# Performance work log

Hardware: AMD Instinct MI355X
Metric: run time of the kernel (lower is better)

The kernel has to match this reference:

```python
import jax, jax.numpy as jnp
import numpy as np

N_NODES = 8192


def _gcn_norm(edge_index, num_nodes):
    # PyG GCNConv default: add self-loops, symmetric normalization.
    src, dst = edge_index[0], edge_index[1]
    loop = jnp.arange(num_nodes, dtype=src.dtype)
    src = jnp.concatenate([src, loop])
    dst = jnp.concatenate([dst, loop])
    deg = jax.ops.segment_sum(jnp.ones_like(dst, dtype=jnp.float32), dst,
                              num_segments=num_nodes)
    dis = jnp.where(deg > 0, jax.lax.rsqrt(jnp.maximum(deg, 1.0)), 0.0)
    norm = dis[src] * dis[dst]  # [E + N]
    return src, dst, norm


def _gcn_conv(x, W, b, src, dst, norm, num_nodes):
    h = x @ W                           # [N, F_out] dense GEMM
    msg = h[src] * norm[:, None]        # gather + scale, [E+N, F_out]
    out = jax.ops.segment_sum(msg, dst, num_segments=num_nodes)  # scatter-add
    return out + b


def setup_inputs() -> dict:
    key = jax.random.key(0)
    ks = jax.random.split(key, 8)
    N, E, F_in, H1, H2, F_out = N_NODES, 65536, 512, 4096, 1024, 10
    x = jax.random.normal(ks[0], (N, F_in), dtype=jnp.float32)
    edge_index = jax.random.randint(ks[1], (2, E), 0, N, dtype=jnp.int64)
    # Glorot-ish scaled weights
    W1 = jax.random.normal(ks[2], (F_in, H1), dtype=jnp.float32) * (1.0 / np.sqrt(F_in))
    b1 = jnp.zeros((H1,), dtype=jnp.float32)
    W2 = jax.random.normal(ks[3], (H1, H2), dtype=jnp.float32) * (1.0 / np.sqrt(H1))
    b2 = jnp.zeros((H2,), dtype=jnp.float32)
    W3 = jax.random.normal(ks[4], (H2, F_out), dtype=jnp.float32) * (1.0 / np.sqrt(H2))
    b3 = jnp.zeros((F_out,), dtype=jnp.float32)
    return {"x": x, "W1": W1, "b1": b1, "W2": W2, "b2": b2,
            "W3": W3, "b3": b3, "edge_index": edge_index}


def reference(x, W1, b1, W2, b2, W3, b3, edge_index):
    N = N_NODES
    src, dst, norm = _gcn_norm(edge_index, N)
    h = _gcn_conv(x.astype(jnp.float32), W1, b1, src, dst, norm, N)
    h = jax.nn.relu(h)  # dropout is identity in eval mode
    h = _gcn_conv(h, W2, b2, src, dst, norm, N)
    h = jax.nn.relu(h)
    h = _gcn_conv(h, W3, b3, src, dst, norm, N)
    return jax.nn.log_softmax(h, axis=1)
```

## Files before the change

kernel.cpp:

```cpp
#include <hip/hip_runtime.h>
#include <math.h>

#define N_NODES 8192
#define N_EDGES 65536
#define F_IN    512
#define HID1    4096
#define HID2    1024
#define F_OUT   10
#define H3_STRIDE 16
#define W3B_STRIDE 1032

typedef __bf16 bf16x8 __attribute__((ext_vector_type(8)));
typedef float floatx4 __attribute__((ext_vector_type(4)));
typedef float floatx16 __attribute__((ext_vector_type(16)));

static __device__ __forceinline__ unsigned short f2bf(float f) {
    union { float f; unsigned u; } v; v.f = f;
    unsigned r = v.u + 0x7fffu + ((v.u >> 16) & 1u);
    return (unsigned short)(r >> 16);
}
static __device__ __forceinline__ float bf2f(unsigned short u) {
    union { unsigned u; float f; } v; v.u = ((unsigned)u) << 16;
    return v.f;
}
static __device__ __forceinline__ void unpack8(uint4 r, float* f) {
    union { unsigned u; float v; } c;
    c.u = r.x << 16;          f[0] = c.v;
    c.u = r.x & 0xffff0000u;  f[1] = c.v;
    c.u = r.y << 16;          f[2] = c.v;
    c.u = r.y & 0xffff0000u;  f[3] = c.v;
    c.u = r.z << 16;          f[4] = c.v;
    c.u = r.z & 0xffff0000u;  f[5] = c.v;
    c.u = r.w << 16;          f[6] = c.v;
    c.u = r.w & 0xffff0000u;  f[7] = c.v;
}
static __device__ __forceinline__ uint4 pack8(const float* f) {
    uint4 o;
    o.x = (unsigned)f2bf(f[0]) | ((unsigned)f2bf(f[1]) << 16);
    o.y = (unsigned)f2bf(f[2]) | ((unsigned)f2bf(f[3]) << 16);
    o.z = (unsigned)f2bf(f[4]) | ((unsigned)f2bf(f[5]) << 16);
    o.w = (unsigned)f2bf(f[6]) | ((unsigned)f2bf(f[7]) << 16);
    return o;
}

__global__ __launch_bounds__(1024) void hist_scan_kernel(
        const int* __restrict__ ei, int* __restrict__ deg,
        int* __restrict__ row_ptr, int* __restrict__ cnt) {
    __shared__ int hist[N_NODES];
    __shared__ int sums[1024];
    int t = threadIdx.x;
#pragma unroll
    for (int i = 0; i < 8; i++) hist[t + i * 1024] = 0;
    __syncthreads();
    const int4* ei4 = (const int4*)(ei + N_EDGES);
#pragma unroll
    for (int i = 0; i < 16; i++) {
        int4 d4 = ei4[i * 1024 + t];
        atomicAdd(&hist[d4.x], 1);
        atomicAdd(&hist[d4.y], 1);
        atomicAdd(&hist[d4.z], 1);
        atomicAdd(&hist[d4.w], 1);
    }
    __syncthreads();
    int base = t * 8;
    int local[8], run = 0;
#pragma unroll
    for (int i = 0; i < 8; i++) {
        int dv = hist[base + i];
        deg[base + i] = dv;
        cnt[base + i] = 0;
        local[i] = run; run += dv;
    }
    sums[t] = run;
    __syncthreads();
    for (int off = 1; off < 1024; off <<= 1) {
        int val = (t >= off) ? sums[t - off] : 0;
        __syncthreads();
        sums[t] += val;
        __syncthreads();
    }
    int offset = (t == 0) ? 0 : sums[t - 1];
#pragma unroll
    for (int i = 0; i < 8; i++) row_ptr[base + i] = offset + local[i];
    if (t == 1023) row_ptr[N_NODES] = sums[1023];
}

static __device__ __forceinline__ void transpose_body(
        const float* __restrict__ W, unsigned short* __restrict__ Wt,
        int K, int N, int k0, int n0, int tid, float (*t)[33]) {
    int c = tid & 31, r8 = tid >> 5;
#pragma unroll
    for (int i = 0; i < 4; i++) {
        int r = r8 + i * 8;
        t[r][c] = W[(size_t)(k0 + r) * N + n0 + c];
    }
    __syncthreads();
#pragma unroll
    for (int i = 0; i < 4; i++) {
        int r = r8 + i * 8;
        Wt[(size_t)(n0 + r) * K + k0 + c] = f2bf(t[c][r]);
    }
}

__global__ __launch_bounds__(256) void megaprep_kernel(
        const int* __restrict__ ei, const int* __restrict__ deg,
        const int* __restrict__ row_ptr, int* __restrict__ cnt,
        int* __restrict__ csr_src, float* __restrict__ csr_w,
        const float* __restrict__ x, unsigned short* __restrict__ xb,
        const float* __restrict__ W1, unsigned short* __restrict__ W1t,
        const float* __restrict__ W2, unsigned short* __restrict__ W2t,
        const float* __restrict__ W3, unsigned short* __restrict__ w3b) {
    __shared__ float t[32][33];
    int b = blockIdx.x, tid = threadIdx.x;
    if (b < 256) {
        int e = b * 256 + tid;
        int s = ei[e];
        int d = ei[N_EDGES + e];
        int slot = row_ptr[d] + atomicAdd(&cnt[d], 1);
        csr_src[slot] = s;
        csr_w[slot] = rsqrtf((float)((deg[s] + 1) * (deg[d] + 1)));
    } else if (b < 4352) {
        int i = (b - 256) * 256 + tid;
        float4 a = ((const float4*)x)[i];
        ushort4 o;
        o.x = f2bf(a.x); o.y = f2bf(a.y); o.z = f2bf(a.z); o.w = f2bf(a.w);
        ((ushort4*)xb)[i] = o;
    } else if (b < 6400) {
        int bb = b - 4352;
        transpose_body(W1, W1t, F_IN, HID1, (bb >> 7) * 32, (bb & 127) * 32, tid, t);
    } else if (b < 10496) {
        int bb = b - 6400;
        transpose_body(W2, W2t, HID1, HID2, (bb >> 5) * 32, (bb & 31) * 32, tid, t);
    } else {
        for (int i = tid; i < HID2 * F_OUT; i += 256) {
            int k = i / F_OUT, c = i % F_OUT;
            w3b[c * W3B_STRIDE + k] = f2bf(W3[i]);
        }
    }
}

__global__ __launch_bounds__(256) void agg1_kernel(
        const unsigned short* __restrict__ xb, const int* __restrict__ row_ptr,
        const int* __restrict__ csr_src, const float* __restrict__ csr_w,
        const int* __restrict__ deg, unsigned short* __restrict__ out) {
    int v = blockIdx.x * 4 + (threadIdx.x >> 6);
    int t = threadIdx.x & 63;
    const uint4* xp = (const uint4*)xb;
    float sw = 1.0f / (float)(deg[v] + 1);
    float acc[8], tmp[8];
    unpack8(xp[(size_t)v * 64 + t], tmp);
#pragma unroll
    for (int j = 0; j < 8; j++) acc[j] = sw * tmp[j];
    int e = row_ptr[v], end = row_ptr[v + 1];
    for (; e + 4 <= end; e += 4) {
        int s0 = csr_src[e], s1 = csr_src[e + 1];
        int s2 = csr_src[e + 2], s3 = csr_src[e + 3];
        float w0 = csr_w[e], w1 = csr_w[e + 1];
        float w2 = csr_w[e + 2], w3 = csr_w[e + 3];
        float f0[8], f1[8], f2[8], f3[8];
        unpack8(xp[(size_t)s0 * 64 + t], f0);
        unpack8(xp[(size_t)s1 * 64 + t], f1);
        unpack8(xp[(size_t)s2 * 64 + t], f2);
        unpack8(xp[(size_t)s3 * 64 + t], f3);
#pragma unroll
        for (int j = 0; j < 8; j++)
            acc[j] += w0 * f0[j] + w1 * f1[j] + w2 * f2[j] + w3 * f3[j];
    }
    for (; e < end; e++) {
        int s = csr_src[e];
        float w = csr_w[e];
        float f0[8];
        unpack8(xp[(size_t)s * 64 + t], f0);
#pragma unroll
        for (int j = 0; j < 8; j++) acc[j] += w * f0[j];
    }
    ((uint4*)out)[(size_t)v * 64 + t] = pack8(acc);
}

__global__ __launch_bounds__(256) void agg2_gemm3_kernel(
        const unsigned short* __restrict__ h, const int* __restrict__ row_ptr,
        const int* __restrict__ csr_src, const float* __restrict__ csr_w,
        const int* __restrict__ deg, const float* __restrict__ b2,
        const unsigned short* __restrict__ w3b, float* __restrict__ H3) {
    __shared__ unsigned short w3s[F_OUT * W3B_STRIDE];
    __shared__ float red[4][F_OUT];
    int tid = threadIdx.x;
    for (int i = tid; i < F_OUT * W3B_STRIDE; i += 256) w3s[i] = w3b[i];
    __syncthreads();
    int half = tid >> 7;
    int t = tid & 127;
    int v = blockIdx.x * 2 + half;
    const uint4* hp = (const uint4*)h;
    float sw = 1.0f / (float)(deg[v] + 1);
    float acc[8], tmp[8];
    unpack8(hp[(size_t)v * 128 + t], tmp);
#pragma unroll
    for (int j = 0; j < 8; j++) acc[j] = sw * tmp[j];
    int e = row_ptr[v], end = row_ptr[v + 1];
    for (; e + 4 <= end; e += 4) {
        int s0 = csr_src[e], s1 = csr_src[e + 1];
        int s2 = csr_src[e + 2], s3 = csr_src[e + 3];
        float w0 = csr_w[e], w1 = csr_w[e + 1];
        float w2 = csr_w[e + 2], w3 = csr_w[e + 3];
        float f0[8], f1[8], f2[8], f3[8];
        unpack8(hp[(size_t)s0 * 128 + t], f0);
        unpack8(hp[(size_t)s1 * 128 + t], f1);
        unpack8(hp[(size_t)s2 * 128 + t], f2);
        unpack8(hp[(size_t)s3 * 128 + t], f3);
#pragma unroll
        for (int j = 0; j < 8; j++)
            acc[j] += w0 * f0[j] + w1 * f1[j] + w2 * f2[j] + w3 * f3[j];
    }
    for (; e < end; e++) {
        int s = csr_src[e];
        float w = csr_w[e];
        float f0[8];
        unpack8(hp[(size_t)s * 128 + t], f0);
#pragma unroll
        for (int j = 0; j < 8; j++) acc[j] += w * f0[j];
    }
    float4 b4a = ((const float4*)b2)[t * 2];
    float4 b4b = ((const float4*)b2)[t * 2 + 1];
    acc[0] = fmaxf(acc[0] + b4a.x, 0.0f); acc[1] = fmaxf(acc[1] + b4a.y, 0.0f);
    acc[2] = fmaxf(acc[2] + b4a.z, 0.0f); acc[3] = fmaxf(acc[3] + b4a.w, 0.0f);
    acc[4] = fmaxf(acc[4] + b4b.x, 0.0f); acc[5] = fmaxf(acc[5] + b4b.y, 0.0f);
    acc[6] = fmaxf(acc[6] + b4b.z, 0.0f); acc[7] = fmaxf(acc[7] + b4b.w, 0.0f);

    float partial[F_OUT];
#pragma unroll
    for (int c = 0; c < F_OUT; c++) {
        float wf[8];
        unpack8(*(const uint4*)&w3s[c * W3B_STRIDE + t * 8], wf);
        partial[c] = acc[0] * wf[0] + acc[1] * wf[1] + acc[2] * wf[2] + acc[3] * wf[3]
                   + acc[4] * wf[4] + acc[5] * wf[5] + acc[6] * wf[6] + acc[7] * wf[7];
    }
#pragma unroll
    for (int c = 0; c < F_OUT; c++) {
#pragma unroll
        for (int off = 32; off > 0; off >>= 1)
            partial[c] += __shfl_xor(partial[c], off, 64);
    }
    int wave = tid >> 6, lane = tid & 63;
    if (lane == 0) {
#pragma unroll
        for (int c = 0; c < F_OUT; c++) red[wave][c] = partial[c];
    }
    __syncthreads();
    if (tid < 2 * F_OUT) {
        int hh = tid / F_OUT, c = tid % F_OUT;
        H3[(size_t)(blockIdx.x * 2 + hh) * H3_STRIDE + c] =
            red[hh * 2][c] + red[hh * 2 + 1][c];
    }
}

#define P8_OFF(R_, lc_) ((((R_) >> 2) * 128) + (((((R_) & 3) << 2) | (lc_)) ^ (((R_) >> 2) & 3)) * 8)

#define Q4_STAGE(Lbuf_, base_, k0_) do {                                       \
    unsigned short* L_ = (Lbuf_);                                              \
    _Pragma("unroll")                                                          \
    for (int j = 0; j < 2; j++) {                                              \
        int sl = j * 512 + tid;                                                \
        int s4 = sl >> 4, cs = sl & 15;                                        \
        int csp = cs ^ (s4 & 3);                                               \
        int grow = s4 * 4 + (csp >> 2);                                        \
        int gcol = (csp & 3) * 8;                                              \
        __builtin_amdgcn_global_load_lds(                                      \
            (const __attribute__((address_space(1))) void*)((base_) + (size_t)grow * K + (k0_) + gcol), \
            (__attribute__((address_space(3))) void*)(&L_[sl * 8]), 16, 0, 0); \
    }                                                                          \
} while (0)

#define P8_STAGE(mat_, kh_, dd_, base_, k0_) \
    Q4_STAGE(lds + ((dd_) * 4 + (mat_) * 2 + (kh_)) * 8192, base_, (k0_) + (kh_) * 32)

#define P8_MAIN_LOOP(NT_)                                                      \
    P8_STAGE(0, 0, 0, Abase, 0);                                               \
    P8_STAGE(1, 0, 0, Bbase, 0);                                               \
    P8_STAGE(0, 1, 0, Abase, 0);                                               \
    P8_STAGE(1, 1, 0, Bbase, 0);                                               \
    asm volatile("s_waitcnt vmcnt(4)" ::: "memory");                           \
    __builtin_amdgcn_s_barrier();                                              \
    for (int t = 0; t < (NT_); t++) {                                          \
        int d = t & 1, dn = d ^ 1;                                             \
        int k1 = (t + 1) * 64;                                                 \
        _Pragma("unroll")                                                      \
        for (int kk = 0; kk < 4; kk++) {                                       \
            if (kk == 2) {                                                     \
                if (t + 1 < (NT_))                                             \
                    asm volatile("s_waitcnt vmcnt(4)" ::: "memory");           \
                else                                                           \
                    asm volatile("s_waitcnt vmcnt(0)" ::: "memory");           \
                __builtin_amdgcn_s_barrier();                                  \
            }                                                                  \
            int kh = kk >> 1;                                                  \
            int lc0 = (kk & 1) * 2 + lhalf;                                    \
            const unsigned short* Ak = lds + (d * 4 + kh) * 8192;              \
            const unsigned short* Bk = lds + (d * 4 + 2 + kh) * 8192;          \
            bf16x8 af[4], bfr[2];                                              \
            _Pragma("unroll")                                                  \
            for (int mt = 0; mt < 4; mt++) {                                   \
                int R = wm * 128 + mt * 32 + lrow;                             \
                af[mt] = *(const bf16x8*)&Ak[P8_OFF(R, lc0)];                  \
            }                                                                  \
            _Pragma("unroll")                                                  \
            for (int nt = 0; nt < 2; nt++) {                                   \
                int R = wn * 64 + nt * 32 + lrow;                              \
                bfr[nt] = *(const bf16x8*)&Bk[P8_OFF(R, lc0)];                 \
            }                                                                  \
            if (t + 1 < (NT_)) {                                               \
                if (kk == 0)      P8_STAGE(0, 0, dn, Abase, k1);               \
                else if (kk == 1) P8_STAGE(1, 0, dn, Bbase, k1);               \
                else if (kk == 2) P8_STAGE(0, 1, dn, Abase, k1);               \
                else              P8_STAGE(1, 1, dn, Bbase, k1);               \
            }                                                                  \
            __builtin_amdgcn_s_barrier();                                      \
            __builtin_amdgcn_s_setprio(1);                                     \
            _Pragma("unroll")                                                  \
            for (int mt = 0; mt < 4; mt++)                                     \
                _Pragma("unroll")                                              \
                for (int nt = 0; nt < 2; nt++)                                 \
                    acc[mt][nt] = __builtin_amdgcn_mfma_f32_32x32x16_bf16(     \
                        af[mt], bfr[nt], acc[mt][nt], 0, 0, 0);                \
            __builtin_amdgcn_s_setprio(0);                                     \
            if (kk == 0 || kk == 2) __builtin_amdgcn_s_barrier();              \
        }                                                                      \
        asm volatile("s_waitcnt vmcnt(4)" ::: "memory");                       \
        __builtin_amdgcn_s_barrier();                                          \
    }

__global__ __launch_bounds__(512, 2) void gemm1_pipe8_kernel(
        const unsigned short* __restrict__ A,
        const unsigned short* __restrict__ Bt,
        const float* __restrict__ bias,
        unsigned short* __restrict__ C) {
    __shared__ unsigned short lds[65536];
    const int K = F_IN, N = HID1;
    int tid = threadIdx.x;
    int wave = tid >> 6, lane = tid & 63;
    int wm = wave >> 2, wn = wave & 3;
    int lrow = lane & 31, lhalf = lane >> 5;

    int b = blockIdx.x;
    int GN = HID1 >> 8;
    int ntile = (b >> 3) % GN;
    int mtile = ((b >> 3) / GN) * 8 + (b & 7);
    int m0 = mtile * 256, n0 = ntile * 256;

    const unsigned short* Abase = A + (size_t)m0 * K;
    const unsigned short* Bbase = Bt + (size_t)n0 * K;

    floatx16 acc[4][2] = {};
    P8_MAIN_LOOP(8)

#pragma unroll
    for (int mt = 0; mt < 4; mt++) {
#pragma unroll
        for (int nt = 0; nt < 2; nt++) {
            int col = n0 + wn * 64 + nt * 32 + lrow;
            float bv = bias[col];
#pragma unroll
            for (int reg = 0; reg < 16; reg++) {
                int row = m0 + wm * 128 + mt * 32 + (reg & 3) + 8 * (reg >> 2) + 4 * lhalf;
                float v = fmaxf(acc[mt][nt][reg] + bv, 0.0f);
                C[(size_t)row * N + col] = f2bf(v);
            }
        }
    }
}

__global__ __launch_bounds__(512, 2) void gemm2_q4v2_split_kernel(
        const unsigned short* __restrict__ A,
        const unsigned short* __restrict__ Bt,
        unsigned short* __restrict__ Ca,
        unsigned short* __restrict__ Cb) {
    __shared__ unsigned short lds[65536];
    const int K = HID1;
    const int N = HID2;
    int tid = threadIdx.x;
    int wave = tid >> 6, lane = tid & 63;
    int wm = wave >> 2, wn = wave & 3;
    int lrow = lane & 31, lhalf = lane >> 5;

    int b = blockIdx.x;
    int u = b >> 3;
    int col = u & 7;
    int mtile = (u >> 3) * 8 + (b & 7);
    int ntile = col >> 1;
    int ksp = col & 1;
    int m0 = mtile * 256, n0 = ntile * 256;
    int koff = ksp * (HID1 / 2);

    const unsigned short* Abase = A + (size_t)m0 * K + koff;
    const unsigned short* Bbase = Bt + (size_t)n0 * K + koff;
    unsigned short* Cout = ksp ? Cb : Ca;

    floatx16 acc[4][2] = {};
    const int NT = (HID1 / 2) >> 5;

    Q4_STAGE(lds + 0 * 16384, Abase, 0);  Q4_STAGE(lds + 0 * 16384 + 8192, Bbase, 0);
    Q4_STAGE(lds + 1 * 16384, Abase, 32); Q4_STAGE(lds + 1 * 16384 + 8192, Bbase, 32);
    Q4_STAGE(lds + 2 * 16384, Abase, 64); Q4_STAGE(lds + 2 * 16384 + 8192, Bbase, 64);
    asm volatile("s_waitcnt vmcnt(8)" ::: "memory");
    __builtin_amdgcn_s_barrier();

    for (int t = 0; t < NT; t++) {
        const unsigned short* Ak = lds + (size_t)(t & 3) * 16384;
        const unsigned short* Bk = Ak + 8192;
        unsigned short* Lnext = lds + (size_t)((t + 3) & 3) * 16384;
        int k3 = (t + 3) * 32;
        if (t + 3 < NT) {
            Q4_STAGE(Lnext, Abase, k3);
            Q4_STAGE(Lnext + 8192, Bbase, k3);
        }
        bf16x8 af[2][4], bfr[2][2];
#pragma unroll
        for (int kk = 0; kk < 2; kk++) {
            int lc0 = kk * 2 + lhalf;
#pragma unroll
            for (int mt = 0; mt < 4; mt++) {
                int R = wm * 128 + mt * 32 + lrow;
                af[kk][mt] = *(const bf16x8*)&Ak[P8_OFF(R, lc0)];
            }
#pragma unroll
            for (int nt = 0; nt < 2; nt++) {
                int R = wn * 64 + nt * 32 + lrow;
                bfr[kk][nt] = *(const bf16x8*)&Bk[P8_OFF(R, lc0)];
            }
        }
        __builtin_amdgcn_s_setprio(1);
#pragma unroll
        for (int kk = 0; kk < 2; kk++)
#pragma unroll
            for (int mt = 0; mt < 4; mt++)
#pragma unroll
                for (int nt = 0; nt < 2; nt++)
                    acc[mt][nt] = __builtin_amdgcn_mfma_f32_32x32x16_bf16(
                        af[kk][mt], bfr[kk][nt], acc[mt][nt], 0, 0, 0);
        __builtin_amdgcn_s_setprio(0);
        if (t + 3 < NT)
            asm volatile("s_waitcnt vmcnt(8)" ::: "memory");
        else if (t + 2 < NT)
            asm volatile("s_waitcnt vmcnt(4)" ::: "memory");
        else if (t + 1 < NT)
            asm volatile("s_waitcnt vmcnt(0)" ::: "memory");
        __builtin_amdgcn_s_barrier();
    }

#pragma unroll
    for (int mt = 0; mt < 4; mt++) {
#pragma unroll
        for (int nt = 0; nt < 2; nt++) {
            int colc = n0 + wn * 64 + nt * 32 + lrow;
#pragma unroll
            for (int reg = 0; reg < 16; reg++) {
                int row = m0 + wm * 128 + mt * 32 + (reg & 3) + 8 * (reg >> 2) + 4 * lhalf;
                Cout[(size_t)row * N + colc] = f2bf(acc[mt][nt][reg]);
            }
        }
    }
}

__global__ __launch_bounds__(256) void merge_kernel(
        const unsigned short* __restrict__ Ca, unsigned short* __restrict__ Cb) {
    const uint4* a4 = (const uint4*)Ca;
    uint4* b4 = (uint4*)Cb;
    int base = blockIdx.x * 1024 + threadIdx.x;
#pragma unroll
    for (int j = 0; j < 4; j++) {
        int i = base + j * 256;
        float fa[8], fb[8];
        unpack8(a4[i], fa);
        unpack8(b4[i], fb);
#pragma unroll
        for (int k = 0; k < 8; k++) fa[k] += fb[k];
        b4[i] = pack8(fa);
    }
}

__global__ void final_kernel(const float* __restrict__ h3, const int* __restrict__ row_ptr,
                             const int* __restrict__ csr_src, const float* __restrict__ csr_w,
                             const int* __restrict__ deg, const float* __restrict__ b3,
                             float* __restrict__ out) {
    int v = blockIdx.x * blockDim.x + threadIdx.x;
    if (v >= N_NODES) return;
    const float4* h4 = (const float4*)h3;
    float sw = 1.0f / (float)(deg[v] + 1);
    float a[12];
    *(float4*)&a[0] = h4[v * 4];
    *(float4*)&a[4] = h4[v * 4 + 1];
    *(float4*)&a[8] = h4[v * 4 + 2];
    float acc[F_OUT];
#pragma unroll
    for (int c = 0; c < F_OUT; c++) acc[c] = b3[c] + sw * a[c];
    int end = row_ptr[v + 1];
    for (int e = row_ptr[v]; e < end; e++) {
        int s = csr_src[e];
        float w = csr_w[e];
        float bsrc[12];
        *(float4*)&bsrc[0] = h4[s * 4];
        *(float4*)&bsrc[4] = h4[s * 4 + 1];
        *(float4*)&bsrc[8] = h4[s * 4 + 2];
#pragma unroll
        for (int c = 0; c < F_OUT; c++) acc[c] += w * bsrc[c];
    }
    float m = acc[0];
#pragma unroll
    for (int c = 1; c < F_OUT; c++) m = fmaxf(m, acc[c]);
    float ssum = 0.0f;
#pragma unroll
    for (int c = 0; c < F_OUT; c++) ssum += expf(acc[c] - m);
    float l = logf(ssum);
#pragma unroll
    for (int c = 0; c < F_OUT; c++) out[v * F_OUT + c] = acc[c] - m - l;
}

extern "C" void kernel_launch(void* const* d_in, const int* in_sizes, int n_in,
                              void* d_out, int out_size, void* d_ws, size_t ws_size,
                              hipStream_t stream) {
    const float* x  = (const float*)d_in[0];
    const float* W1 = (const float*)d_in[1];
    const float* b1 = (const float*)d_in[2];
    const float* W2 = (const float*)d_in[3];
    const float* b2 = (const float*)d_in[4];
    const float* W3 = (const float*)d_in[5];
    const float* b3 = (const float*)d_in[6];
    const int*   ei = (const int*)d_in[7];
    float* out = (float*)d_out;

    char* p = (char*)d_ws;
    int*   deg     = (int*)p;    p += N_NODES * 4;
    int*   cnt     = (int*)p;    p += N_NODES * 4;
    int*   row_ptr = (int*)p;    p += 33024;
    int*   csr_src = (int*)p;    p += N_EDGES * 4;
    float* csr_w   = (float*)p;  p += N_EDGES * 4;
    float* h3      = (float*)p;  p += N_NODES * H3_STRIDE * 4;
    unsigned short* w3b = (unsigned short*)p; p += (F_OUT * W3B_STRIDE * 2 + 255) / 256 * 256;
    unsigned short* xb    = (unsigned short*)p; p += (size_t)N_NODES * F_IN * 2;
    unsigned short* agg_x = (unsigned short*)p; p += (size_t)N_NODES * F_IN * 2;
    unsigned short* W1t   = (unsigned short*)p; p += (size_t)HID1 * F_IN * 2;
    unsigned short* W2t   = (unsigned short*)p; p += (size_t)HID2 * HID1 * 2;
    unsigned short* h1    = (unsigned short*)p; p += (size_t)N_NODES * HID1 * 2;
    unsigned short* h2pre = (unsigned short*)p; p += (size_t)N_NODES * HID2 * 2;
    unsigned short* h2a = xb;

    hist_scan_kernel<<<1, 1024, 0, stream>>>(ei, deg, row_ptr, cnt);
    megaprep_kernel<<<10497, 256, 0, stream>>>(ei, deg, row_ptr, cnt, csr_src, csr_w,
                                               x, xb, W1, W1t, W2, W2t, W3, w3b);

    agg1_kernel<<<N_NODES / 4, 256, 0, stream>>>(xb, row_ptr, csr_src, csr_w, deg, agg_x);
    gemm1_pipe8_kernel<<<(N_NODES / 256) * (HID1 / 256), 512, 0, stream>>>(
        agg_x, W1t, b1, h1);

    gemm2_q4v2_split_kernel<<<256, 512, 0, stream>>>(h1, W2t, h2a, h2pre);
    merge_kernel<<<1024, 256, 0, stream>>>(h2a, h2pre);

    agg2_gemm3_kernel<<<N_NODES / 2, 256, 0, stream>>>(h2pre, row_ptr, csr_src, csr_w,
                                                       deg, b2, w3b, h3);

    final_kernel<<<N_NODES / 256, 256, 0, stream>>>(h3, row_ptr, csr_src, csr_w, deg, b3, out);
}
```

Before: 287.2 us.

## Slice feature dimension in aggregation kernels and interleave GEMM2 prefetch with MFMA

The two gather-aggregation kernels now split each node's feature row into column slices handled by separate blocks. Each lane loads one 32-bit pair instead of a 16-byte vector, which multiplies the number of blocks and the memory-level parallelism for the irregular gathers. The fused layer-3 projection now reads W3 directly into registers, writes per-slice partial sums, and adds a small reduce kernel; this removes the W3 prep and the LDS staging. The GEMM2 loop also issues its next-stage global prefetch inside the kk loop between the fragment loads and the MFMAs to overlap better, at the cost of narrower loads and an extra launch plus partial-sum traffic.

```diff
diff --git a/kernel.cpp b/kernel.cpp
--- a/kernel.cpp
+++ b/kernel.cpp
@@ -8,20 +8,14 @@
 #define HID2    1024
 #define F_OUT   10
 #define H3_STRIDE 16
-#define W3B_STRIDE 1032
 
 typedef __bf16 bf16x8 __attribute__((ext_vector_type(8)));
-typedef float floatx4 __attribute__((ext_vector_type(4)));
 typedef float floatx16 __attribute__((ext_vector_type(16)));
 
 static __device__ __forceinline__ unsigned short f2bf(float f) {
     union { float f; unsigned u; } v; v.f = f;
     unsigned r = v.u + 0x7fffu + ((v.u >> 16) & 1u);
     return (unsigned short)(r >> 16);
-}
-static __device__ __forceinline__ float bf2f(unsigned short u) {
-    union { unsigned u; float f; } v; v.u = ((unsigned)u) << 16;
-    return v.f;
 }
 static __device__ __forceinline__ void unpack8(uint4 r, float* f) {
     union { unsigned u; float v; } c;
@@ -108,8 +102,7 @@
         int* __restrict__ csr_src, float* __restrict__ csr_w,
         const float* __restrict__ x, unsigned short* __restrict__ xb,
         const float* __restrict__ W1, unsigned short* __restrict__ W1t,
-        const float* __restrict__ W2, unsigned short* __restrict__ W2t,
-        const float* __restrict__ W3, unsigned short* __restrict__ w3b) {
+        const float* __restrict__ W2, unsigned short* __restrict__ W2t) {
     __shared__ float t[32][33];
     int b = blockIdx.x, tid = threadIdx.x;
     if (b < 256) {
@@ -128,129 +121,129 @@
     } else if (b < 6400) {
         int bb = b - 4352;
         transpose_body(W1, W1t, F_IN, HID1, (bb >> 7) * 32, (bb & 127) * 32, tid, t);
-    } else if (b < 10496) {
+    } else {
         int bb = b - 6400;
         transpose_body(W2, W2t, HID1, HID2, (bb >> 5) * 32, (bb & 31) * 32, tid, t);
-    } else {
-        for (int i = tid; i < HID2 * F_OUT; i += 256) {
-            int k = i / F_OUT, c = i % F_OUT;
-            w3b[c * W3B_STRIDE + k] = f2bf(W3[i]);
-        }
-    }
-}
-
-__global__ __launch_bounds__(256) void agg1_kernel(
+    }
+}
+
+__global__ __launch_bounds__(256) void agg1_sliced_kernel(
         const unsigned short* __restrict__ xb, const int* __restrict__ row_ptr,
         const int* __restrict__ csr_src, const float* __restrict__ csr_w,
         const int* __restrict__ deg, unsigned short* __restrict__ out) {
-    int v = blockIdx.x * 4 + (threadIdx.x >> 6);
-    int t = threadIdx.x & 63;
-    const uint4* xp = (const uint4*)xb;
+    int b = blockIdx.x;
+    int slice = b & 3;
+    int ng = b >> 2;
+    int v = ng * 4 + (threadIdx.x >> 6);
+    int lane = threadIdx.x & 63;
+    int sbase = slice * 64 + lane;
+    const unsigned* xu = (const unsigned*)xb;
     float sw = 1.0f / (float)(deg[v] + 1);
-    float acc[8], tmp[8];
-    unpack8(xp[(size_t)v * 64 + t], tmp);
-#pragma unroll
-    for (int j = 0; j < 8; j++) acc[j] = sw * tmp[j];
+    union { unsigned u; float f; } cv;
+    unsigned su = xu[(size_t)v * 256 + sbase];
+    float a0, a1;
+    cv.u = su << 16;          a0 = sw * cv.f;
+    cv.u = su & 0xffff0000u;  a1 = sw * cv.f;
     int e = row_ptr[v], end = row_ptr[v + 1];
     for (; e + 4 <= end; e += 4) {
-        int s0 = csr_src[e], s1 = csr_src[e + 1];
+        int s0 = csr_src[e],     s1 = csr_src[e + 1];
         int s2 = csr_src[e + 2], s3 = csr_src[e + 3];
-        float w0 = csr_w[e], w1 = csr_w[e + 1];
+        float w0 = csr_w[e],     w1 = csr_w[e + 1];
         float w2 = csr_w[e + 2], w3 = csr_w[e + 3];
-        float f0[8], f1[8], f2[8], f3[8];
-        unpack8(xp[(size_t)s0 * 64 + t], f0);
-        unpack8(xp[(size_t)s1 * 64 + t], f1);
-        unpack8(xp[(size_t)s2 * 64 + t], f2);
-        unpack8(xp[(size_t)s3 * 64 + t], f3);
-#pragma unroll
-        for (int j = 0; j < 8; j++)
-            acc[j] += w0 * f0[j] + w1 * f1[j] + w2 * f2[j] + w3 * f3[j];
+        unsigned u0 = xu[(size_t)s0 * 256 + sbase];
+        unsigned u1 = xu[(size_t)s1 * 256 + sbase];
+        unsigned u2 = xu[(size_t)s2 * 256 + sbase];
+        unsigned u3 = xu[(size_t)s3 * 256 + sbase];
+        cv.u = u0 << 16; a0 += w0 * cv.f;  cv.u = u0 & 0xffff0000u; a1 += w0 * cv.f;
+        cv.u = u1 << 16; a0 += w1 * cv.f;  cv.u = u1 & 0xffff0000u; a1 += w1 * cv.f;
+        cv.u = u2 << 16; a0 += w2 * cv.f;  cv.u = u2 & 0xffff0000u; a1 += w2 * cv.f;
+        cv.u = u3 << 16; a0 += w3 * cv.f;  cv.u = u3 & 0xffff0000u; a1 += w3 * cv.f;
     }
     for (; e < end; e++) {
-        int s = csr_src[e];
-        float w = csr_w[e];
-        float f0[8];
-        unpack8(xp[(size_t)s * 64 + t], f0);
-#pragma unroll
-        for (int j = 0; j < 8; j++) acc[j] += w * f0[j];
-    }
-    ((uint4*)out)[(size_t)v * 64 + t] = pack8(acc);
-}
-
-__global__ __launch_bounds__(256) void agg2_gemm3_kernel(
+        int s = csr_src[e]; float w = csr_w[e];
+        unsigned u0 = xu[(size_t)s * 256 + sbase];
+        cv.u = u0 << 16; a0 += w * cv.f;  cv.u = u0 & 0xffff0000u; a1 += w * cv.f;
+    }
+    ((unsigned*)out)[(size_t)v * 256 + sbase] =
+        (unsigned)f2bf(a0) | ((unsigned)f2bf(a1) << 16);
+}
+
+__global__ __launch_bounds__(256) void agg2_gemm3_sliced_kernel(
         const unsigned short* __restrict__ h, const int* __restrict__ row_ptr,
         const int* __restrict__ csr_src, const float* __restrict__ csr_w,
         const int* __restrict__ deg, const float* __restrict__ b2,
-        const unsigned short* __restrict__ w3b, float* __restrict__ H3) {
-    __shared__ unsigned short w3s[F_OUT * W3B_STRIDE];
-    __shared__ float red[4][F_OUT];
-    int tid = threadIdx.x;
-    for (int i = tid; i < F_OUT * W3B_STRIDE; i += 256) w3s[i] = w3b[i];
-    __syncthreads();
-    int half = tid >> 7;
-    int t = tid & 127;
-    int v = blockIdx.x * 2 + half;
-    const uint4* hp = (const uint4*)h;
+        const float* __restrict__ W3, float* __restrict__ h3p) {
+    int b = blockIdx.x;
+    int slice = b & 7;
+    int ng = b >> 3;
+    int v = ng * 4 + (threadIdx.x >> 6);
+    int lane = threadIdx.x & 63;
+    int sbase = slice * 64 + lane;
+    int f0 = slice * 128 + lane * 2;
+    const unsigned* hu = (const unsigned*)h;
+    float w3r0[F_OUT], w3r1[F_OUT];
+#pragma unroll
+    for (int c = 0; c < F_OUT; c++) {
+        w3r0[c] = W3[(size_t)f0 * F_OUT + c];
+        w3r1[c] = W3[(size_t)(f0 + 1) * F_OUT + c];
+    }
+    float bv0 = b2[f0], bv1 = b2[f0 + 1];
     float sw = 1.0f / (float)(deg[v] + 1);
-    float acc[8], tmp[8];
-    unpack8(hp[(size_t)v * 128 + t], tmp);
-#pragma unroll
-    for (int j = 0; j < 8; j++) acc[j] = sw * tmp[j];
+    union { unsigned u; float f; } cv;
+    unsigned su = hu[(size_t)v * 512 + sbase];
+    float a0, a1;
+    cv.u = su << 16;          a0 = sw * cv.f;
+    cv.u = su & 0xffff0000u;  a1 = sw * cv.f;
     int e = row_ptr[v], end = row_ptr[v + 1];
     for (; e + 4 <= end; e += 4) {
-        int s0 = csr_src[e], s1 = csr_src[e + 1];
+        int s0 = csr_src[e],     s1 = csr_src[e + 1];
         int s2 = csr_src[e + 2], s3 = csr_src[e + 3];
-        float w0 = csr_w[e], w1 = csr_w[e + 1];
+        float w0 = csr_w[e],     w1 = csr_w[e + 1];
         float w2 = csr_w[e + 2], w3 = csr_w[e + 3];
-        float f0[8], f1[8], f2[8], f3[8];
-        unpack8(hp[(size_t)s0 * 128 + t], f0);
-        unpack8(hp[(size_t)s1 * 128 + t], f1);
-        unpack8(hp[(size_t)s2 * 128 + t], f2);
-        unpack8(hp[(size_t)s3 * 128 + t], f3);
-#pragma unroll
-        for (int j = 0; j < 8; j++)
-            acc[j] += w0 * f0[j] + w1 * f1[j] + w2 * f2[j] + w3 * f3[j];
+        unsigned u0 = hu[(size_t)s0 * 512 + sbase];
+        unsigned u1 = hu[(size_t)s1 * 512 + sbase];
+        unsigned u2 = hu[(size_t)s2 * 512 + sbase];
+        unsigned u3 = hu[(size_t)s3 * 512 + sbase];
+        cv.u = u0 << 16; a0 += w0 * cv.f;  cv.u = u0 & 0xffff0000u; a1 += w0 * cv.f;
+        cv.u = u1 << 16; a0 += w1 * cv.f;  cv.u = u1 & 0xffff0000u; a1 += w1 * cv.f;
+        cv.u = u2 << 16; a0 += w2 * cv.f;  cv.u = u2 & 0xffff0000u; a1 += w2 * cv.f;
+        cv.u = u3 << 16; a0 += w3 * cv.f;  cv.u = u3 & 0xffff0000u; a1 += w3 * cv.f;
     }
     for (; e < end; e++) {
-        int s = csr_src[e];
-        float w = csr_w[e];
-        float f0[8];
-        unpack8(hp[(size_t)s * 128 + t], f0);
-#pragma unroll
-        for (int j = 0; j < 8; j++) acc[j] += w * f0[j];
-    }
-    float4 b4a = ((const float4*)b2)[t * 2];
-    float4 b4b = ((const float4*)b2)[t * 2 + 1];
-    acc[0] = fmaxf(acc[0] + b4a.x, 0.0f); acc[1] = fmaxf(acc[1] + b4a.y, 0.0f);
-    acc[2] = fmaxf(acc[2] + b4a.z, 0.0f); acc[3] = fmaxf(acc[3] + b4a.w, 0.0f);
-    acc[4] = fmaxf(acc[4] + b4b.x, 0.0f); acc[5] = fmaxf(acc[5] + b4b.y, 0.0f);
-    acc[6] = fmaxf(acc[6] + b4b.z, 0.0f); acc[7] = fmaxf(acc[7] + b4b.w, 0.0f);
-
+        int s = csr_src[e]; float w = csr_w[e];
+        unsigned u0 = hu[(size_t)s * 512 + sbase];
+        cv.u = u0 << 16; a0 += w * cv.f;  cv.u = u0 & 0xffff0000u; a1 += w * cv.f;
+    }
+    a0 = fmaxf(a0 + bv0, 0.0f);
+    a1 = fmaxf(a1 + bv1, 0.0f);
     float partial[F_OUT];
 #pragma unroll
-    for (int c = 0; c < F_OUT; c++) {
-        float wf[8];
-        unpack8(*(const uint4*)&w3s[c * W3B_STRIDE + t * 8], wf);
-        partial[c] = acc[0] * wf[0] + acc[1] * wf[1] + acc[2] * wf[2] + acc[3] * wf[3]
-                   + acc[4] * wf[4] + acc[5] * wf[5] + acc[6] * wf[6] + acc[7] * wf[7];
-    }
+    for (int c = 0; c < F_OUT; c++) partial[c] = a0 * w3r0[c] + a1 * w3r1[c];
 #pragma unroll
     for (int c = 0; c < F_OUT; c++) {
 #pragma unroll
         for (int off = 32; off > 0; off >>= 1)
             partial[c] += __shfl_xor(partial[c], off, 64);
     }
-    int wave = tid >> 6, lane = tid & 63;
     if (lane == 0) {
-#pragma unroll
-        for (int c = 0; c < F_OUT; c++) red[wave][c] = partial[c];
-    }
-    __syncthreads();
-    if (tid < 2 * F_OUT) {
-        int hh = tid / F_OUT, c = tid % F_OUT;
-        H3[(size_t)(blockIdx.x * 2 + hh) * H3_STRIDE + c] =
-            red[hh * 2][c] + red[hh * 2 + 1][c];
-    }
+        float* dst = h3p + ((size_t)slice * N_NODES + v) * H3_STRIDE;
+#pragma unroll
+        for (int c = 0; c < F_OUT; c++) dst[c] = partial[c];
+    }
+}
+
+__global__ __launch_bounds__(256) void reduce_h3_kernel(
+        const float* __restrict__ h3p, float* __restrict__ h3) {
+    int idx = blockIdx.x * 256 + threadIdx.x;
+    int v = idx >> 2, g = idx & 3;
+    const float4* p4 = (const float4*)h3p;
+    float4 s = make_float4(0.f, 0.f, 0.f, 0.f);
+#pragma unroll
+    for (int sl = 0; sl < 8; sl++) {
+        float4 a = p4[((size_t)sl * N_NODES + v) * 4 + g];
+        s.x += a.x; s.y += a.y; s.z += a.z; s.w += a.w;
+    }
+    ((float4*)h3)[(size_t)v * 4 + g] = s;
 }
 
 #define P8_OFF(R_, lc_) ((((R_) >> 2) * 128) + (((((R_) & 3) << 2) | (lc_)) ^ (((R_) >> 2) & 3)) * 8)
@@ -368,7 +361,7 @@
     }
 }
 
-__global__ __launch_bounds__(512, 2) void gemm2_q4v2_split_kernel(
+__global__ __launch_bounds__(512, 2) void gemm2_q4_split_kernel(
         const unsigned short* __restrict__ A,
         const unsigned short* __restrict__ Bt,
         unsigned short* __restrict__ Ca,
@@ -408,35 +401,33 @@
         const unsigned short* Bk = Ak + 8192;
         unsigned short* Lnext = lds + (size_t)((t + 3) & 3) * 16384;
         int k3 = (t + 3) * 32;
-        if (t + 3 < NT) {
-            Q4_STAGE(Lnext, Abase, k3);
-            Q4_STAGE(Lnext + 8192, Bbase, k3);
-        }
-        bf16x8 af[2][4], bfr[2][2];
 #pragma unroll
         for (int kk = 0; kk < 2; kk++) {
             int lc0 = kk * 2 + lhalf;
+            bf16x8 af[4], bfr[2];
 #pragma unroll
             for (int mt = 0; mt < 4; mt++) {
                 int R = wm * 128 + mt * 32 + lrow;
-                af[kk][mt] = *(const bf16x8*)&Ak[P8_OFF(R, lc0)];
+                af[mt] = *(const bf16x8*)&Ak[P8_OFF(R, lc0)];
             }
 #pragma unroll
             for (int nt = 0; nt < 2; nt++) {
                 int R = wn * 64 + nt * 32 + lrow;
-                bfr[kk][nt] = *(const bf16x8*)&Bk[P8_OFF(R, lc0)];
+                bfr[nt] = *(const bf16x8*)&Bk[P8_OFF(R, lc0)];
             }
-        }
-        __builtin_amdgcn_s_setprio(1);
-#pragma unroll
-        for (int kk = 0; kk < 2; kk++)
+            if (t + 3 < NT) {
+                if (kk == 0) Q4_STAGE(Lnext, Abase, k3);
+                else         Q4_STAGE(Lnext + 8192, Bbase, k3);
+            }
+            __builtin_amdgcn_s_setprio(1);
 #pragma unroll
             for (int mt = 0; mt < 4; mt++)
 #pragma unroll
                 for (int nt = 0; nt < 2; nt++)
                     acc[mt][nt] = __builtin_amdgcn_mfma_f32_32x32x16_bf16(
-                        af[kk][mt], bfr[kk][nt], acc[mt][nt], 0, 0, 0);
-        __builtin_amdgcn_s_setprio(0);
+                        af[mt], bfr[nt], acc[mt][nt], 0, 0, 0);
+            __builtin_amdgcn_s_setprio(0);
+        }
         if (t + 3 < NT)
             asm volatile("s_waitcnt vmcnt(8)" ::: "memory");
         else if (t + 2 < NT)
@@ -534,7 +525,6 @@
     int*   csr_src = (int*)p;    p += N_EDGES * 4;
     float* csr_w   = (float*)p;  p += N_EDGES * 4;
     float* h3      = (float*)p;  p += N_NODES * H3_STRIDE * 4;
-    unsigned short* w3b = (unsigned short*)p; p += (F_OUT * W3B_STRIDE * 2 + 255) / 256 * 256;
     unsigned short* xb    = (unsigned short*)p; p += (size_t)N_NODES * F_IN * 2;
     unsigned short* agg_x = (unsigned short*)p; p += (size_t)N_NODES * F_IN * 2;
     unsigned short* W1t   = (unsigned short*)p; p += (size_t)HID1 * F_IN * 2;
@@ -542,20 +532,23 @@
     unsigned short* h1    = (unsigned short*)p; p += (size_t)N_NODES * HID1 * 2;
     unsigned short* h2pre = (unsigned short*)p; p += (size_t)N_NODES * HID2 * 2;
     unsigned short* h2a = xb;
+    float* h3p = (float*)xb;
 
     hist_scan_kernel<<<1, 1024, 0, stream>>>(ei, deg, row_ptr, cnt);
-    megaprep_kernel<<<10497, 256, 0, stream>>>(ei, deg, row_ptr, cnt, csr_src, csr_w,
-                                               x, xb, W1, W1t, W2, W2t, W3, w3b);
-
-    agg1_kernel<<<N_NODES / 4, 256, 0, stream>>>(xb, row_ptr, csr_src, csr_w, deg, agg_x);
+    megaprep_kernel<<<10496, 256, 0, stream>>>(ei, deg, row_ptr, cnt, csr_src, csr_w,
+                                               x, xb, W1, W1t, W2, W2t);
+
+    agg1_sliced_kernel<<<N_NODES / 4 * 4, 256, 0, stream>>>(
+        xb, row_ptr, csr_src, csr_w, deg, agg_x);
     gemm1_pipe8_kernel<<<(N_NODES / 256) * (HID1 / 256), 512, 0, stream>>>(
         agg_x, W1t, b1, h1);
 
-    gemm2_q4v2_split_kernel<<<256, 512, 0, stream>>>(h1, W2t, h2a, h2pre);
+    gemm2_q4_split_kernel<<<256, 512, 0, stream>>>(h1, W2t, h2a, h2pre);
     merge_kernel<<<1024, 256, 0, stream>>>(h2a, h2pre);
 
-    agg2_gemm3_kernel<<<N_NODES / 2, 256, 0, stream>>>(h2pre, row_ptr, csr_src, csr_w,
-                                                       deg, b2, w3b, h3);
+    agg2_gemm3_sliced_kernel<<<N_NODES / 4 * 8, 256, 0, stream>>>(
+        h2pre, row_ptr, csr_src, csr_w, deg, b2, W3, h3p);
+    reduce_h3_kernel<<<N_NODES * 4 / 256, 256, 0, stream>>>(h3p, h3);
 
     final_kernel<<<N_NODES / 256, 256, 0, stream>>>(h3, row_ptr, csr_src, csr_w, deg, b3, out);
 }
```

Result: no change. 291.2 us, median of 2 (+1.4%).
